# Performance work log

Hardware: AMD Instinct MI355X
Metric: run time of the kernel (lower is better)

## Reference

```python
import jax, jax.numpy as jnp
import numpy as np
from jax import lax

N_NODES = 50000
N_EDGES = 800000
FEAT = 16
HID = 64
K = 32
N_CLASSES = 8


def _dconv(Xc, W, b, src, dst, norm_out, norm_in):
    """Dual-direction diffusion (Chebyshev-style) graph convolution.
    Xc: [N, Fin], W: [2, K, Fin, HID], norm_*: per-edge weights."""
    N = Xc.shape[0]

    def prop(x, s, d, ne):
        # out[i] = sum_{e: d[e]=i} ne[e] * x[s[e]]
        return jax.ops.segment_sum(x[s] * ne[:, None], d, num_segments=N)

    # k = 0 term (identity support, both directions)
    H = Xc @ (W[0, 0] + W[1, 0])
    # k = 1 term
    T1o = prop(Xc, src, dst, norm_out)   # forward diffusion
    T1i = prop(Xc, dst, src, norm_in)    # reverse diffusion
    H = H + T1o @ W[0, 1] + T1i @ W[1, 1]

    def step(carry, Wk):
        T0o, T1o, T0i, T1i, Hacc = carry
        T2o = 2.0 * prop(T1o, src, dst, norm_out) - T0o
        T2i = 2.0 * prop(T1i, dst, src, norm_in) - T0i
        Hacc = Hacc + T2o @ Wk[0] + T2i @ Wk[1]
        return (T1o, T2o, T1i, T2i, Hacc), None

    Wtail = jnp.stack([W[0, 2:], W[1, 2:]], axis=1)  # [K-2, 2, Fin, HID]
    (_, _, _, _, H), _ = lax.scan(step, (Xc, T1o, Xc, T1i, H), Wtail)
    return H + b


def setup_inputs() -> dict:
    key = jax.random.key(0)
    ks = jax.random.split(key, 8)
    Fin = FEAT + HID
    wscale = 1.0 / np.sqrt(Fin * K)
    x = jax.random.normal(ks[0], (N_NODES, FEAT), jnp.float32)
    edge_index = jax.random.randint(ks[1], (2, N_EDGES), 0, N_NODES, jnp.int64)
    W_z = jax.random.normal(ks[2], (2, K, Fin, HID), jnp.float32) * wscale
    W_r = jax.random.normal(ks[3], (2, K, Fin, HID), jnp.float32) * wscale
    W_h = jax.random.normal(ks[4], (2, K, Fin, HID), jnp.float32) * wscale
    lin_w = jax.random.normal(ks[5], (HID, N_CLASSES), jnp.float32) / np.sqrt(HID)
    return {
        "x": x, "edge_index": edge_index,
        "W_z": W_z, "b_z": jnp.zeros((HID,), jnp.float32),
        "W_r": W_r, "b_r": jnp.zeros((HID,), jnp.float32),
        "W_h": W_h, "b_h": jnp.zeros((HID,), jnp.float32),
        "lin_w": lin_w, "lin_b": jnp.zeros((N_CLASSES,), jnp.float32),
    }


def reference(x, edge_index, W_z, b_z, W_r, b_r, W_h, b_h, lin_w, lin_b):
    N = x.shape[0]
    src, dst = edge_index[0], edge_index[1]
    w = jnp.ones(src.shape[0], x.dtype)
    deg_out = jax.ops.segment_sum(w, src, num_segments=N)
    deg_in = jax.ops.segment_sum(w, dst, num_segments=N)
    inv = lambda d: jnp.where(d > 0, 1.0 / d, 0.0)
    norm_out = inv(deg_out)[src]  # per-edge 1/out-deg(source), forward walk
    norm_in = inv(deg_in)[dst]    # per-edge 1/in-deg(target), reverse walk

    # DCRNN GRU cell, single step, H initialized to zeros
    H0 = jnp.zeros((N, HID), x.dtype)
    Xc = jnp.concatenate([x, H0], axis=1)
    Z = jax.nn.sigmoid(_dconv(Xc, W_z, b_z, src, dst, norm_out, norm_in))
    R = jax.nn.sigmoid(_dconv(Xc, W_r, b_r, src, dst, norm_out, norm_in))
    Xh = jnp.concatenate([x, H0 * R], axis=1)
    Ht = jnp.tanh(_dconv(Xh, W_h, b_h, src, dst, norm_out, norm_in))
    H = Z * H0 + (1.0 - Z) * Ht

    return jax.nn.relu(H) @ lin_w + lin_b
```

## Files before the change

kernel.cpp:

```cpp
#include <hip/hip_runtime.h>
#include <math.h>

#define N_NODES 50000
#define N_EDGES 800000
#define FEAT    16
#define HID     64
#define KORD    32
#define NCLS    8

#define WSL     5120
#define SLOT    (N_NODES * FEAT)

typedef __attribute__((ext_vector_type(8))) short bf8_t;
typedef __attribute__((ext_vector_type(4))) float f32x4;

static constexpr size_t Aln(size_t x) { return (x + 255) & ~size_t(255); }

static constexpr size_t OFF_DEG_OUT = 0;
static constexpr size_t OFF_DEG_IN  = OFF_DEG_OUT + Aln(N_NODES * 4);
static constexpr size_t OFF_CUR_DST = OFF_DEG_IN  + Aln(N_NODES * 4);
static constexpr size_t OFF_CUR_SRC = OFF_CUR_DST + Aln(N_NODES * 4);
static constexpr size_t ZERO_BYTES  = OFF_CUR_SRC + Aln(N_NODES * 4);
static constexpr size_t OFF_OFF_DST = ZERO_BYTES;
static constexpr size_t OFF_OFF_SRC = OFF_OFF_DST + Aln((N_NODES + 1) * 4);
static constexpr size_t OFF_CSRD    = OFF_OFF_SRC + Aln((N_NODES + 1) * 4);
static constexpr size_t OFF_CSRS    = OFF_CSRD + Aln(N_EDGES * 4);
static constexpr size_t OFF_SLAB    = OFF_CSRS + Aln(N_EDGES * 4);
static constexpr size_t OFF_BSZH    = OFF_SLAB + Aln((size_t)64 * SLOT * 4);
static constexpr size_t OFF_BSZL    = OFF_BSZH + Aln((size_t)32 * 8 * 64 * 8 * 2);
static constexpr size_t WS_TOTAL    = OFF_BSZL + Aln((size_t)32 * 8 * 64 * 8 * 2);

__device__ __forceinline__ ushort f2bf(float v) {
    unsigned int b = __float_as_uint(v);
    b += 0x7FFFu + ((b >> 16) & 1u);
    return (ushort)(b >> 16);
}
__device__ __forceinline__ float bf2f(ushort h) {
    return __uint_as_float((unsigned int)h << 16);
}

__global__ void count_deg_kernel(const int* __restrict__ ei,
                                 int* __restrict__ deg_out, int* __restrict__ deg_in) {
    int e4 = blockIdx.x * blockDim.x + threadIdx.x;
    if (e4 * 4 >= N_EDGES) return;
    int4 s = *(const int4*)&ei[e4 * 4];
    int4 d = *(const int4*)&ei[N_EDGES + e4 * 4];
    atomicAdd(&deg_out[s.x], 1); atomicAdd(&deg_out[s.y], 1);
    atomicAdd(&deg_out[s.z], 1); atomicAdd(&deg_out[s.w], 1);
    atomicAdd(&deg_in[d.x], 1);  atomicAdd(&deg_in[d.y], 1);
    atomicAdd(&deg_in[d.z], 1);  atomicAdd(&deg_in[d.w], 1);
}

__global__ __launch_bounds__(1024) void scan_kernel(const int* __restrict__ degA, int* __restrict__ offA,
                                                    const int* __restrict__ degB, int* __restrict__ offB) {
    const int* deg = blockIdx.x ? degB : degA;
    int* off = blockIdx.x ? offB : offA;
    __shared__ int wsum[16];
    __shared__ int s_run;
    const int t = threadIdx.x, lane = t & 63, wid = t >> 6;
    if (t == 0) s_run = 0;
    __syncthreads();
    for (int base = 0; base < N_NODES; base += 1024) {
        int i = base + t;
        int v = (i < N_NODES) ? deg[i] : 0;
        int xv = v;
        #pragma unroll
        for (int d = 1; d < 64; d <<= 1) {
            int tt = __shfl_up(xv, d, 64);
            if (lane >= d) xv += tt;
        }
        if (lane == 63) wsum[wid] = xv;
        __syncthreads();
        int add = s_run;
        for (int w = 0; w < wid; ++w) add += wsum[w];
        if (i < N_NODES) off[i] = add + xv - v;
        __syncthreads();
        if (t == 1023) s_run = add + xv;
        __syncthreads();
    }
    if (t == 0) off[N_NODES] = s_run;
}

__global__ void fill_csr_kernel(const int* __restrict__ ei,
                                const int* __restrict__ deg_out, const int* __restrict__ deg_in,
                                const int* __restrict__ off_dst, const int* __restrict__ off_src,
                                int* __restrict__ cur_dst, int* __restrict__ cur_src,
                                unsigned int* __restrict__ csrd, unsigned int* __restrict__ csrs) {
    int e = blockIdx.x * blockDim.x + threadIdx.x;
    if (e >= N_EDGES) return;
    int s = ei[e], d = ei[N_EDGES + e];
    int p = off_dst[d] + atomicAdd(&cur_dst[d], 1);
    csrd[p] = ((unsigned int)deg_out[s] << 16) | (unsigned int)s;
    int q = off_src[s] + atomicAdd(&cur_src[s], 1);
    csrs[q] = ((unsigned int)deg_in[d] << 16) | (unsigned int)d;
}

__device__ __forceinline__ float4 gather4d(const unsigned int* __restrict__ csr, int beg, int end,
                                           int u, int fq, const float* __restrict__ src) {
    float4 acc = {0.f, 0.f, 0.f, 0.f};
    for (int e0 = beg; e0 < end; e0 += 16) {
        int ea = e0 + u, eb = e0 + 4 + u, ec = e0 + 8 + u, ed = e0 + 12 + u;
        unsigned int pa = (ea < end) ? csr[ea] : 0x10000u;
        unsigned int pb = (eb < end) ? csr[eb] : 0x10000u;
        unsigned int pc = (ec < end) ? csr[ec] : 0x10000u;
        unsigned int pd = (ed < end) ? csr[ed] : 0x10000u;
        float wa = (ea < end) ? 1.0f / (float)(pa >> 16) : 0.0f;
        float wb = (eb < end) ? 1.0f / (float)(pb >> 16) : 0.0f;
        float wc = (ec < end) ? 1.0f / (float)(pc >> 16) : 0.0f;
        float wd = (ed < end) ? 1.0f / (float)(pd >> 16) : 0.0f;
        const float4 ra = *(const float4*)&src[(pa & 0xFFFFu) * FEAT + fq * 4];
        const float4 rb = *(const float4*)&src[(pb & 0xFFFFu) * FEAT + fq * 4];
        const float4 rc = *(const float4*)&src[(pc & 0xFFFFu) * FEAT + fq * 4];
        const float4 rd = *(const float4*)&src[(pd & 0xFFFFu) * FEAT + fq * 4];
        acc.x += wa * ra.x + wb * rb.x + wc * rc.x + wd * rd.x;
        acc.y += wa * ra.y + wb * rb.y + wc * rc.y + wd * rd.y;
        acc.z += wa * ra.z + wb * rb.z + wc * rc.z + wd * rd.z;
        acc.w += wa * ra.w + wb * rb.w + wc * rc.w + wd * rd.w;
    }
    return acc;
}

__device__ __forceinline__ float4 reduce_u(float4 a) {
    a.x += __shfl_xor(a.x, 4); a.y += __shfl_xor(a.y, 4);
    a.z += __shfl_xor(a.z, 4); a.w += __shfl_xor(a.w, 4);
    a.x += __shfl_xor(a.x, 8); a.y += __shfl_xor(a.y, 8);
    a.z += __shfl_xor(a.z, 8); a.w += __shfl_xor(a.w, 8);
    return a;
}

__global__ __launch_bounds__(256) void init_kernel(
    const float* __restrict__ x,
    const int* __restrict__ off_dst, const unsigned int* __restrict__ csrd,
    const int* __restrict__ off_src, const unsigned int* __restrict__ csrs,
    float* __restrict__ slab) {
    const int dir = blockIdx.y;
    const int* off = dir ? off_src : off_dst;
    const unsigned int* csr = dir ? csrs : csrd;
    const int t = threadIdx.x;
    const int g = t >> 4, l = t & 15, u = l >> 2, fq = l & 3;
    const int i = blockIdx.x * 16 + g;
    const int b = off[i], e = off[i + 1];
    float4 a = reduce_u(gather4d(csr, b, e, u, fq, x));
    if (u == 0) {
        const int ro = i * FEAT + fq * 4;
        float4 xr = *(const float4*)&x[ro];
        *(float4*)&slab[(size_t)(dir * 32 + 0) * SLOT + ro] = xr;
        *(float4*)&slab[(size_t)(dir * 32 + 1) * SLOT + ro] = a;
    }
}

__global__ __launch_bounds__(256) void step_kernel(
    const int* __restrict__ off_dst, const unsigned int* __restrict__ csrd,
    const int* __restrict__ off_src, const unsigned int* __restrict__ csrs,
    float* __restrict__ slab, int k) {
    const int dir = blockIdx.y;
    const int* off = dir ? off_src : off_dst;
    const unsigned int* csr = dir ? csrs : csrd;
    const float* prev = slab + (size_t)(dir * 32 + k - 1) * SLOT;
    const float* pp   = slab + (size_t)(dir * 32 + k - 2) * SLOT;
    float*       outp = slab + (size_t)(dir * 32 + k) * SLOT;
    const int t = threadIdx.x;
    const int g = t >> 4, l = t & 15, u = l >> 2, fq = l & 3;
    const int i = blockIdx.x * 16 + g;
    const int b = off[i], e = off[i + 1];
    float4 a = reduce_u(gather4d(csr, b, e, u, fq, prev));
    if (u == 0) {
        const int ro = i * FEAT + fq * 4;
        float4 p = *(const float4*)&pp[ro];
        float4 t2;
        t2.x = 2.f * a.x - p.x; t2.y = 2.f * a.y - p.y;
        t2.z = 2.f * a.z - p.z; t2.w = 2.f * a.w - p.w;
        *(float4*)&outp[ro] = t2;
    }
}

__global__ void wswiz_kernel(const float* __restrict__ Wz, const float* __restrict__ Wh,
                             ushort* __restrict__ bszh, ushort* __restrict__ bszl) {
    int idx = blockIdx.x * blockDim.x + threadIdx.x;
    if (idx >= 32 * 8 * 64) return;
    int l  = idx & 63;
    int nc = (idx >> 6) & 7;
    int kc = idx >> 9;
    int si = kc * 2 + ((l >> 4) >> 1);
    int f0 = ((l >> 4) & 1) * 8;
    int c  = nc * 16 + (l & 15);
    const float* W = (c < 64) ? Wz : Wh;
    int cc = (c < 64) ? c : c - 64;
    ushort vh[8], vl[8];
    #pragma unroll
    for (int i = 0; i < 8; ++i) {
        float v = W[(size_t)si * WSL + (f0 + i) * 64 + cc];
        ushort h = f2bf(v);
        vh[i] = h;
        vl[i] = f2bf(v - bf2f(h));
    }
    ushort* dh = &bszh[(size_t)idx * 8];
    *(ushort4*)dh       = make_ushort4(vh[0], vh[1], vh[2], vh[3]);
    *(ushort4*)(dh + 4) = make_ushort4(vh[4], vh[5], vh[6], vh[7]);
    ushort* dl = &bszl[(size_t)idx * 8];
    *(ushort4*)dl       = make_ushort4(vl[0], vl[1], vl[2], vl[3]);
    *(ushort4*)(dl + 4) = make_ushort4(vl[4], vl[5], vl[6], vl[7]);
}

__global__ __launch_bounds__(256) void final_kernel(
    const float* __restrict__ slab, const ushort* __restrict__ bszh, const ushort* __restrict__ bszl,
    const float* __restrict__ bz, const float* __restrict__ bh,
    const float* __restrict__ lin_w, const float* __restrict__ lin_b,
    float* __restrict__ out) {
    const int t = threadIdx.x;
    const int w = t >> 6, l = t & 63;
    const int cl = l & 15, hi = l >> 4;
    const int n0 = blockIdx.x * 64 + w * 16;

    f32x4 acc[8];
    #pragma unroll
    for (int nc = 0; nc < 8; ++nc) {
        int c = nc * 16 + cl;
        float bias = (c < 64) ? bz[c] : bh[c - 64];
        acc[nc] = (f32x4){bias, bias, bias, bias};
    }

    const int nodeA = n0 + cl;
    const int aOk = (nodeA < N_NODES);
    const int siAdd = (hi >> 1);
    const int f0 = (hi & 1) * 8;

    for (int kc = 0; kc < 32; ++kc) {
        bf8_t aHi = (bf8_t)0, aLo = (bf8_t)0;
        if (aOk) {
            int si = kc * 2 + siAdd;
            const float* ap = &slab[(size_t)si * SLOT + nodeA * FEAT + f0];
            float4 a0 = *(const float4*)ap;
            float4 a1 = *(const float4*)(ap + 4);
            float av[8] = {a0.x, a0.y, a0.z, a0.w, a1.x, a1.y, a1.z, a1.w};
            #pragma unroll
            for (int i = 0; i < 8; ++i) {
                ushort h = f2bf(av[i]);
                aHi[i] = (short)h;
                aLo[i] = (short)f2bf(av[i] - bf2f(h));
            }
        }
        #pragma unroll
        for (int nc = 0; nc < 8; ++nc) {
            const size_t fo = (size_t)(((kc * 8 + nc) * 64) + l) * 8;
            bf8_t bHi = *(const bf8_t*)&bszh[fo];
            bf8_t bLo = *(const bf8_t*)&bszl[fo];
            acc[nc] = __builtin_amdgcn_mfma_f32_16x16x32_bf16(aHi, bHi, acc[nc], 0, 0, 0);
            acc[nc] = __builtin_amdgcn_mfma_f32_16x16x32_bf16(aLo, bHi, acc[nc], 0, 0, 0);
            acc[nc] = __builtin_amdgcn_mfma_f32_16x16x32_bf16(aHi, bLo, acc[nc], 0, 0, 0);
        }
    }

    float po[4][8];
    #pragma unroll
    for (int i = 0; i < 4; ++i)
        #pragma unroll
        for (int cls = 0; cls < 8; ++cls) po[i][cls] = 0.f;
    #pragma unroll
    for (int i = 0; i < 4; ++i) {
        #pragma unroll
        for (int nc = 0; nc < 4; ++nc) {
            float hz = acc[nc][i], hh = acc[nc + 4][i];
            float z  = 1.f / (1.f + __expf(-hz));
            float ht = tanhf(hh);
            float v  = fmaxf(0.f, (1.f - z) * ht);
            const float* lwr = &lin_w[(nc * 16 + cl) * 8];
            #pragma unroll
            for (int cls = 0; cls < 8; ++cls) po[i][cls] += v * lwr[cls];
        }
    }
    #pragma unroll
    for (int m = 1; m < 16; m <<= 1) {
        #pragma unroll
        for (int i = 0; i < 4; ++i)
            #pragma unroll
            for (int cls = 0; cls < 8; ++cls)
                po[i][cls] += __shfl_xor(po[i][cls], m, 16);
    }
    if (cl < 8) {
        #pragma unroll
        for (int i = 0; i < 4; ++i) {
            int node = n0 + hi * 4 + i;
            if (node < N_NODES) out[node * NCLS + cl] = po[i][cl] + lin_b[cl];
        }
    }
}

extern "C" void kernel_launch(void* const* d_in, const int* in_sizes, int n_in,
                              void* d_out, int out_size, void* d_ws, size_t ws_size,
                              hipStream_t stream) {
    const float* x   = (const float*)d_in[0];
    const int*   ei  = (const int*)d_in[1];
    const float* Wz  = (const float*)d_in[2];
    const float* bz  = (const float*)d_in[3];
    const float* Wh  = (const float*)d_in[6];
    const float* bh  = (const float*)d_in[7];
    const float* lw  = (const float*)d_in[8];
    const float* lb  = (const float*)d_in[9];
    float* out = (float*)d_out;
    char* ws = (char*)d_ws;

    int*  deg_out = (int*)(ws + OFF_DEG_OUT);
    int*  deg_in  = (int*)(ws + OFF_DEG_IN);
    int*  cur_dst = (int*)(ws + OFF_CUR_DST);
    int*  cur_src = (int*)(ws + OFF_CUR_SRC);
    int*  off_dst = (int*)(ws + OFF_OFF_DST);
    int*  off_src = (int*)(ws + OFF_OFF_SRC);
    unsigned int* csrd = (unsigned int*)(ws + OFF_CSRD);
    unsigned int* csrs = (unsigned int*)(ws + OFF_CSRS);
    float*  slab = (float*)(ws + OFF_SLAB);
    ushort* bszh = (ushort*)(ws + OFF_BSZH);
    ushort* bszl = (ushort*)(ws + OFF_BSZL);

    hipMemsetAsync(ws, 0, ZERO_BYTES, stream);

    const int EB = (N_EDGES + 255) / 256;
    const int NB16 = N_NODES / 16;
    count_deg_kernel<<<(N_EDGES / 4 + 255) / 256, 256, 0, stream>>>(ei, deg_out, deg_in);
    scan_kernel<<<2, 1024, 0, stream>>>(deg_in, off_dst, deg_out, off_src);
    fill_csr_kernel<<<EB, 256, 0, stream>>>(ei, deg_out, deg_in, off_dst, off_src,
                                            cur_dst, cur_src, csrd, csrs);
    wswiz_kernel<<<(32 * 8 * 64 + 255) / 256, 256, 0, stream>>>(Wz, Wh, bszh, bszl);
    init_kernel<<<dim3(NB16, 2), 256, 0, stream>>>(x, off_dst, csrd, off_src, csrs, slab);

    for (int k = 2; k < KORD; ++k)
        step_kernel<<<dim3(NB16, 2), 256, 0, stream>>>(off_dst, csrd, off_src, csrs, slab, k);

    final_kernel<<<(N_NODES + 63) / 64, 256, 0, stream>>>(slab, bszh, bszl, bz, bh, lw, lb, out);
}
```

Baseline: 849.5 us.

## Store degree-prescaled Chebyshev terms, shrink CSR to 16-bit indices, split final K-reduction

Every Chebyshev term is now stored pre-divided by its node's degree. The gather then only sums neighbours with no per-edge weight or division, and the CSR holds plain 16-bit indices, which halves index bandwidth. The step kernel rescales to keep the recurrence exact, and the final kernel multiplies the degree back in before the MFMA projection. The final kernel also splits the 32 orders across 4 waves per 16-node block and reduces through shared memory, adding an LDS round trip and a sync. Multiplying and dividing by the degree can add small rounding differences.

```diff
diff --git a/kernel.cpp b/kernel.cpp
--- a/kernel.cpp
+++ b/kernel.cpp
@@ -24,8 +24,8 @@
 static constexpr size_t OFF_OFF_DST = ZERO_BYTES;
 static constexpr size_t OFF_OFF_SRC = OFF_OFF_DST + Aln((N_NODES + 1) * 4);
 static constexpr size_t OFF_CSRD    = OFF_OFF_SRC + Aln((N_NODES + 1) * 4);
-static constexpr size_t OFF_CSRS    = OFF_CSRD + Aln(N_EDGES * 4);
-static constexpr size_t OFF_SLAB    = OFF_CSRS + Aln(N_EDGES * 4);
+static constexpr size_t OFF_CSRS    = OFF_CSRD + Aln(N_EDGES * 2);
+static constexpr size_t OFF_SLAB    = OFF_CSRS + Aln(N_EDGES * 2);
 static constexpr size_t OFF_BSZH    = OFF_SLAB + Aln((size_t)64 * SLOT * 4);
 static constexpr size_t OFF_BSZL    = OFF_BSZH + Aln((size_t)32 * 8 * 64 * 8 * 2);
 static constexpr size_t WS_TOTAL    = OFF_BSZL + Aln((size_t)32 * 8 * 64 * 8 * 2);
@@ -82,40 +82,39 @@
 }
 
 __global__ void fill_csr_kernel(const int* __restrict__ ei,
-                                const int* __restrict__ deg_out, const int* __restrict__ deg_in,
                                 const int* __restrict__ off_dst, const int* __restrict__ off_src,
                                 int* __restrict__ cur_dst, int* __restrict__ cur_src,
-                                unsigned int* __restrict__ csrd, unsigned int* __restrict__ csrs) {
+                                ushort* __restrict__ csrd, ushort* __restrict__ csrs) {
     int e = blockIdx.x * blockDim.x + threadIdx.x;
     if (e >= N_EDGES) return;
     int s = ei[e], d = ei[N_EDGES + e];
     int p = off_dst[d] + atomicAdd(&cur_dst[d], 1);
-    csrd[p] = ((unsigned int)deg_out[s] << 16) | (unsigned int)s;
+    csrd[p] = (ushort)s;
     int q = off_src[s] + atomicAdd(&cur_src[s], 1);
-    csrs[q] = ((unsigned int)deg_in[d] << 16) | (unsigned int)d;
-}
-
-__device__ __forceinline__ float4 gather4d(const unsigned int* __restrict__ csr, int beg, int end,
+    csrs[q] = (ushort)d;
+}
+
+__device__ __forceinline__ float4 gather_s(const ushort* __restrict__ csr, int beg, int end,
                                            int u, int fq, const float* __restrict__ src) {
     float4 acc = {0.f, 0.f, 0.f, 0.f};
     for (int e0 = beg; e0 < end; e0 += 16) {
         int ea = e0 + u, eb = e0 + 4 + u, ec = e0 + 8 + u, ed = e0 + 12 + u;
-        unsigned int pa = (ea < end) ? csr[ea] : 0x10000u;
-        unsigned int pb = (eb < end) ? csr[eb] : 0x10000u;
-        unsigned int pc = (ec < end) ? csr[ec] : 0x10000u;
-        unsigned int pd = (ed < end) ? csr[ed] : 0x10000u;
-        float wa = (ea < end) ? 1.0f / (float)(pa >> 16) : 0.0f;
-        float wb = (eb < end) ? 1.0f / (float)(pb >> 16) : 0.0f;
-        float wc = (ec < end) ? 1.0f / (float)(pc >> 16) : 0.0f;
-        float wd = (ed < end) ? 1.0f / (float)(pd >> 16) : 0.0f;
-        const float4 ra = *(const float4*)&src[(pa & 0xFFFFu) * FEAT + fq * 4];
-        const float4 rb = *(const float4*)&src[(pb & 0xFFFFu) * FEAT + fq * 4];
-        const float4 rc = *(const float4*)&src[(pc & 0xFFFFu) * FEAT + fq * 4];
-        const float4 rd = *(const float4*)&src[(pd & 0xFFFFu) * FEAT + fq * 4];
-        acc.x += wa * ra.x + wb * rb.x + wc * rc.x + wd * rd.x;
-        acc.y += wa * ra.y + wb * rb.y + wc * rc.y + wd * rd.y;
-        acc.z += wa * ra.z + wb * rb.z + wc * rc.z + wd * rd.z;
-        acc.w += wa * ra.w + wb * rb.w + wc * rc.w + wd * rd.w;
+        int ia = (ea < end) ? (int)csr[ea] : 0;
+        int ib = (eb < end) ? (int)csr[eb] : 0;
+        int ic = (ec < end) ? (int)csr[ec] : 0;
+        int id = (ed < end) ? (int)csr[ed] : 0;
+        float ma = (ea < end) ? 1.0f : 0.0f;
+        float mb = (eb < end) ? 1.0f : 0.0f;
+        float mc = (ec < end) ? 1.0f : 0.0f;
+        float md = (ed < end) ? 1.0f : 0.0f;
+        const float4 ra = *(const float4*)&src[ia * FEAT + fq * 4];
+        const float4 rb = *(const float4*)&src[ib * FEAT + fq * 4];
+        const float4 rc = *(const float4*)&src[ic * FEAT + fq * 4];
+        const float4 rd = *(const float4*)&src[id * FEAT + fq * 4];
+        acc.x += ma * ra.x + mb * rb.x + mc * rc.x + md * rd.x;
+        acc.y += ma * ra.y + mb * rb.y + mc * rc.y + md * rd.y;
+        acc.z += ma * ra.z + mb * rb.z + mc * rc.z + md * rd.z;
+        acc.w += ma * ra.w + mb * rb.w + mc * rc.w + md * rd.w;
     }
     return acc;
 }
@@ -128,34 +127,54 @@
     return a;
 }
 
+__global__ void scale_x_kernel(const float* __restrict__ x,
+                               const int* __restrict__ deg_out, const int* __restrict__ deg_in,
+                               float* __restrict__ slab) {
+    int q = blockIdx.x * blockDim.x + threadIdx.x;
+    if (q * 4 >= SLOT) return;
+    int node = q >> 2;
+    float invO = 1.0f / (float)(deg_out[node] > 0 ? deg_out[node] : 1);
+    float invI = 1.0f / (float)(deg_in[node]  > 0 ? deg_in[node]  : 1);
+    float4 v = *(const float4*)&x[q * 4];
+    float4 o = {v.x * invO, v.y * invO, v.z * invO, v.w * invO};
+    float4 ii = {v.x * invI, v.y * invI, v.z * invI, v.w * invI};
+    *(float4*)&slab[(size_t)0 * SLOT + q * 4] = o;
+    *(float4*)&slab[(size_t)32 * SLOT + q * 4] = ii;
+}
+
 __global__ __launch_bounds__(256) void init_kernel(
-    const float* __restrict__ x,
-    const int* __restrict__ off_dst, const unsigned int* __restrict__ csrd,
-    const int* __restrict__ off_src, const unsigned int* __restrict__ csrs,
+    const int* __restrict__ off_dst, const ushort* __restrict__ csrd,
+    const int* __restrict__ off_src, const ushort* __restrict__ csrs,
+    const int* __restrict__ deg_out, const int* __restrict__ deg_in,
     float* __restrict__ slab) {
     const int dir = blockIdx.y;
     const int* off = dir ? off_src : off_dst;
-    const unsigned int* csr = dir ? csrs : csrd;
+    const ushort* csr = dir ? csrs : csrd;
+    const int* dga = dir ? deg_in : deg_out;
+    const float* src = slab + (size_t)(dir * 32) * SLOT;
+    float* outp = slab + (size_t)(dir * 32 + 1) * SLOT;
     const int t = threadIdx.x;
     const int g = t >> 4, l = t & 15, u = l >> 2, fq = l & 3;
     const int i = blockIdx.x * 16 + g;
     const int b = off[i], e = off[i + 1];
-    float4 a = reduce_u(gather4d(csr, b, e, u, fq, x));
+    float4 a = reduce_u(gather_s(csr, b, e, u, fq, src));
     if (u == 0) {
         const int ro = i * FEAT + fq * 4;
-        float4 xr = *(const float4*)&x[ro];
-        *(float4*)&slab[(size_t)(dir * 32 + 0) * SLOT + ro] = xr;
-        *(float4*)&slab[(size_t)(dir * 32 + 1) * SLOT + ro] = a;
+        float inv = 1.0f / (float)(dga[i] > 0 ? dga[i] : 1);
+        float4 t2 = {a.x * inv, a.y * inv, a.z * inv, a.w * inv};
+        *(float4*)&outp[ro] = t2;
     }
 }
 
 __global__ __launch_bounds__(256) void step_kernel(
-    const int* __restrict__ off_dst, const unsigned int* __restrict__ csrd,
-    const int* __restrict__ off_src, const unsigned int* __restrict__ csrs,
+    const int* __restrict__ off_dst, const ushort* __restrict__ csrd,
+    const int* __restrict__ off_src, const ushort* __restrict__ csrs,
+    const int* __restrict__ deg_out, const int* __restrict__ deg_in,
     float* __restrict__ slab, int k) {
     const int dir = blockIdx.y;
     const int* off = dir ? off_src : off_dst;
-    const unsigned int* csr = dir ? csrs : csrd;
+    const ushort* csr = dir ? csrs : csrd;
+    const int* dga = dir ? deg_in : deg_out;
     const float* prev = slab + (size_t)(dir * 32 + k - 1) * SLOT;
     const float* pp   = slab + (size_t)(dir * 32 + k - 2) * SLOT;
     float*       outp = slab + (size_t)(dir * 32 + k) * SLOT;
@@ -163,13 +182,17 @@
     const int g = t >> 4, l = t & 15, u = l >> 2, fq = l & 3;
     const int i = blockIdx.x * 16 + g;
     const int b = off[i], e = off[i + 1];
-    float4 a = reduce_u(gather4d(csr, b, e, u, fq, prev));
+    float4 a = reduce_u(gather_s(csr, b, e, u, fq, prev));
     if (u == 0) {
         const int ro = i * FEAT + fq * 4;
+        float dv = (float)(dga[i] > 0 ? dga[i] : 1);
+        float inv = 1.0f / dv;
         float4 p = *(const float4*)&pp[ro];
         float4 t2;
-        t2.x = 2.f * a.x - p.x; t2.y = 2.f * a.y - p.y;
-        t2.z = 2.f * a.z - p.z; t2.w = 2.f * a.w - p.w;
+        t2.x = (2.f * a.x - p.x * dv) * inv;
+        t2.y = (2.f * a.y - p.y * dv) * inv;
+        t2.z = (2.f * a.z - p.z * dv) * inv;
+        t2.w = (2.f * a.w - p.w * dv) * inv;
         *(float4*)&outp[ro] = t2;
     }
 }
@@ -204,41 +227,46 @@
 
 __global__ __launch_bounds__(256) void final_kernel(
     const float* __restrict__ slab, const ushort* __restrict__ bszh, const ushort* __restrict__ bszl,
+    const int* __restrict__ deg_out, const int* __restrict__ deg_in,
     const float* __restrict__ bz, const float* __restrict__ bh,
     const float* __restrict__ lin_w, const float* __restrict__ lin_b,
     float* __restrict__ out) {
+    __shared__ float red[3][64][33];
     const int t = threadIdx.x;
     const int w = t >> 6, l = t & 63;
     const int cl = l & 15, hi = l >> 4;
-    const int n0 = blockIdx.x * 64 + w * 16;
+    const int n0 = blockIdx.x * 16;
 
     f32x4 acc[8];
     #pragma unroll
     for (int nc = 0; nc < 8; ++nc) {
-        int c = nc * 16 + cl;
-        float bias = (c < 64) ? bz[c] : bh[c - 64];
+        float bias = 0.f;
+        if (w == 0) {
+            int c = nc * 16 + cl;
+            bias = (c < 64) ? bz[c] : bh[c - 64];
+        }
         acc[nc] = (f32x4){bias, bias, bias, bias};
     }
 
     const int nodeA = n0 + cl;
-    const int aOk = (nodeA < N_NODES);
     const int siAdd = (hi >> 1);
     const int f0 = (hi & 1) * 8;
-
-    for (int kc = 0; kc < 32; ++kc) {
-        bf8_t aHi = (bf8_t)0, aLo = (bf8_t)0;
-        if (aOk) {
-            int si = kc * 2 + siAdd;
-            const float* ap = &slab[(size_t)si * SLOT + nodeA * FEAT + f0];
-            float4 a0 = *(const float4*)ap;
-            float4 a1 = *(const float4*)(ap + 4);
-            float av[8] = {a0.x, a0.y, a0.z, a0.w, a1.x, a1.y, a1.z, a1.w};
-            #pragma unroll
-            for (int i = 0; i < 8; ++i) {
-                ushort h = f2bf(av[i]);
-                aHi[i] = (short)h;
-                aLo[i] = (short)f2bf(av[i] - bf2f(h));
-            }
+    const int* dga = (w >= 2) ? deg_in : deg_out;
+    const float dF = (float)(dga[nodeA] > 0 ? dga[nodeA] : 1);
+
+    for (int kc = w * 8; kc < w * 8 + 8; ++kc) {
+        int si = kc * 2 + siAdd;
+        const float* ap = &slab[(size_t)si * SLOT + nodeA * FEAT + f0];
+        float4 a0 = *(const float4*)ap;
+        float4 a1 = *(const float4*)(ap + 4);
+        float av[8] = {a0.x * dF, a0.y * dF, a0.z * dF, a0.w * dF,
+                       a1.x * dF, a1.y * dF, a1.z * dF, a1.w * dF};
+        bf8_t aHi, aLo;
+        #pragma unroll
+        for (int i = 0; i < 8; ++i) {
+            ushort h = f2bf(av[i]);
+            aHi[i] = (short)h;
+            aLo[i] = (short)f2bf(av[i] - bf2f(h));
         }
         #pragma unroll
         for (int nc = 0; nc < 8; ++nc) {
@@ -250,6 +278,23 @@
             acc[nc] = __builtin_amdgcn_mfma_f32_16x16x32_bf16(aHi, bLo, acc[nc], 0, 0, 0);
         }
     }
+
+    if (w > 0) {
+        #pragma unroll
+        for (int nc = 0; nc < 8; ++nc)
+            #pragma unroll
+            for (int i = 0; i < 4; ++i)
+                red[w - 1][l][nc * 4 + i] = acc[nc][i];
+    }
+    __syncthreads();
+    if (w != 0) return;
+    #pragma unroll
+    for (int r = 0; r < 3; ++r)
+        #pragma unroll
+        for (int nc = 0; nc < 8; ++nc)
+            #pragma unroll
+            for (int i = 0; i < 4; ++i)
+                acc[nc][i] += red[r][l][nc * 4 + i];
 
     float po[4][8];
     #pragma unroll
@@ -281,7 +326,7 @@
         #pragma unroll
         for (int i = 0; i < 4; ++i) {
             int node = n0 + hi * 4 + i;
-            if (node < N_NODES) out[node * NCLS + cl] = po[i][cl] + lin_b[cl];
+            out[node * NCLS + cl] = po[i][cl] + lin_b[cl];
         }
     }
 }
@@ -306,11 +351,11 @@
     int*  cur_src = (int*)(ws + OFF_CUR_SRC);
     int*  off_dst = (int*)(ws + OFF_OFF_DST);
     int*  off_src = (int*)(ws + OFF_OFF_SRC);
-    unsigned int* csrd = (unsigned int*)(ws + OFF_CSRD);
-    unsigned int* csrs = (unsigned int*)(ws + OFF_CSRS);
-    float*  slab = (float*)(ws + OFF_SLAB);
-    ushort* bszh = (ushort*)(ws + OFF_BSZH);
-    ushort* bszl = (ushort*)(ws + OFF_BSZL);
+    ushort* csrd  = (ushort*)(ws + OFF_CSRD);
+    ushort* csrs  = (ushort*)(ws + OFF_CSRS);
+    float*  slab  = (float*)(ws + OFF_SLAB);
+    ushort* bszh  = (ushort*)(ws + OFF_BSZH);
+    ushort* bszl  = (ushort*)(ws + OFF_BSZL);
 
     hipMemsetAsync(ws, 0, ZERO_BYTES, stream);
 
@@ -318,13 +363,17 @@
     const int NB16 = N_NODES / 16;
     count_deg_kernel<<<(N_EDGES / 4 + 255) / 256, 256, 0, stream>>>(ei, deg_out, deg_in);
     scan_kernel<<<2, 1024, 0, stream>>>(deg_in, off_dst, deg_out, off_src);
-    fill_csr_kernel<<<EB, 256, 0, stream>>>(ei, deg_out, deg_in, off_dst, off_src,
+    fill_csr_kernel<<<EB, 256, 0, stream>>>(ei, off_dst, off_src,
                                             cur_dst, cur_src, csrd, csrs);
     wswiz_kernel<<<(32 * 8 * 64 + 255) / 256, 256, 0, stream>>>(Wz, Wh, bszh, bszl);
-    init_kernel<<<dim3(NB16, 2), 256, 0, stream>>>(x, off_dst, csrd, off_src, csrs, slab);
+    scale_x_kernel<<<(SLOT / 4 + 255) / 256, 256, 0, stream>>>(x, deg_out, deg_in, slab);
+    init_kernel<<<dim3(NB16, 2), 256, 0, stream>>>(off_dst, csrd, off_src, csrs,
+                                                   deg_out, deg_in, slab);
 
     for (int k = 2; k < KORD; ++k)
-        step_kernel<<<dim3(NB16, 2), 256, 0, stream>>>(off_dst, csrd, off_src, csrs, slab, k);
-
-    final_kernel<<<(N_NODES + 63) / 64, 256, 0, stream>>>(slab, bszh, bszl, bz, bh, lw, lb, out);
-}
+        step_kernel<<<dim3(NB16, 2), 256, 0, stream>>>(off_dst, csrd, off_src, csrs,
+                                                       deg_out, deg_in, slab, k);
+
+    final_kernel<<<NB16, 256, 0, stream>>>(slab, bszh, bszl, deg_out, deg_in,
+                                           bz, bh, lw, lb, out);
+}
```

Measured after the change: 991.6 us. 16.7% more time.
